# Optimization experiments

Hardware: AMD Instinct MI355X
Metric: run time of the kernel (lower is better)

The kernel has to match this reference:

```python
import jax, jax.numpy as jnp
import numpy as np

N_NODES = 100000


def _gcn_conv(x, W, b, src, dst, n):
    # PyG GCNConv (default): add self-loops, norm = deg^{-1/2}[src] * deg^{-1/2}[dst]
    # degree computed on target nodes (col) with unit edge weights, then
    # out[i] = sum_{(j->i)} norm_ji * (x_j @ W) + b
    loops = jnp.arange(n, dtype=src.dtype)
    s = jnp.concatenate([src, loops])
    d = jnp.concatenate([dst, loops])
    deg = jax.ops.segment_sum(jnp.ones_like(d, dtype=x.dtype), d, num_segments=n)
    dinv = jnp.where(deg > 0, jax.lax.rsqrt(deg), 0.0)
    h = x @ W                                  # [n, out_dim]
    norm = (dinv[s] * dinv[d])[:, None]        # [E+n, 1]
    msg = h[s] * norm                          # gather + scale
    out = jax.ops.segment_sum(msg, d, num_segments=n)  # scatter-add to targets
    return out + b


def setup_inputs() -> dict:
    key = jax.random.key(0)
    ks = jax.random.split(key, 4)
    x = jax.random.normal(ks[0], (N_NODES, 128), dtype=jnp.float32)
    edge_index = jax.random.randint(ks[1], (2, 1600000), 0, N_NODES, dtype=jnp.int64)
    W1 = jax.random.normal(ks[2], (128, 16), dtype=jnp.float32) * (1.0 / np.sqrt(128))
    b1 = jnp.zeros((16,), dtype=jnp.float32)
    W2 = jax.random.normal(ks[3], (16, 3), dtype=jnp.float32) * (1.0 / np.sqrt(16))
    b2 = jnp.zeros((3,), dtype=jnp.float32)
    return {"x": x, "edge_index": edge_index, "W1": W1, "b1": b1, "W2": W2, "b2": b2}


def reference(x, edge_index, W1, b1, W2, b2):
    src, dst = edge_index[0], edge_index[1]
    n = x.shape[0]
    h = _gcn_conv(x, W1, b1, src, dst, n)
    h = jax.nn.relu(h)
    # F.dropout in eval mode == identity (deterministic baseline)
    h = _gcn_conv(h, W2, b2, src, dst, n)
    return jax.nn.log_softmax(h, axis=1)
```

## Files before the change

### kernel.cpp

```cpp
#include <hip/hip_runtime.h>
#include <hip/hip_fp16.h>
#include <math.h>


#define BSH 9
#define BNODES 512
#define P1 512

struct alignas(8) Half4 { __half x, y, z, w; };

__global__ void k1a_count(const int* __restrict__ dst, int* __restrict__ hist_t,
                          int NBK, int E) {
    __shared__ int lh[256];
    int t = threadIdx.x;
    lh[t] = 0;
    __syncthreads();
    int slice = (E + P1 - 1) / P1;
    int e0 = blockIdx.x * slice, e1 = min(E, e0 + slice);
    for (int e = e0 + t; e < e1; e += 256)
        atomicAdd(&lh[dst[e] >> BSH], 1);
    __syncthreads();
    for (int i = t; i < NBK; i += 256)
        hist_t[(size_t)i * P1 + blockIdx.x] = lh[i];
}

__global__ void kscan1(const int* __restrict__ hist_t, int* __restrict__ colpre_t,
                       int* __restrict__ btot, int NBK) {
    __shared__ int v[P1], part[256];
    int kb = blockIdx.x, t = threadIdx.x;
    v[t] = hist_t[(size_t)kb * P1 + t];
    v[t + 256] = hist_t[(size_t)kb * P1 + t + 256];
    __syncthreads();
    int a = v[2 * t], c = v[2 * t + 1];
    part[t] = a + c;
    __syncthreads();
    for (int o = 1; o < 256; o <<= 1) {
        int add = (t >= o) ? part[t - o] : 0;
        __syncthreads();
        part[t] += add;
        __syncthreads();
    }
    int pre = (t == 0) ? 0 : part[t - 1];
    colpre_t[(size_t)kb * P1 + 2 * t] = pre;
    colpre_t[(size_t)kb * P1 + 2 * t + 1] = pre + a;
    if (t == 255) btot[kb] = part[255];
}

__global__ void kscan2(const int* __restrict__ btot, int* __restrict__ bucket_base, int NBK) {
    __shared__ int s[256];
    int t = threadIdx.x;
    int orig = (t < NBK) ? btot[t] : 0;
    s[t] = orig;
    __syncthreads();
    for (int o = 1; o < 256; o <<= 1) {
        int add = (t >= o) ? s[t - o] : 0;
        __syncthreads();
        s[t] += add;
        __syncthreads();
    }
    if (t < NBK) {
        bucket_base[t] = s[t] - orig;
        if (t == NBK - 1) bucket_base[NBK] = s[t];
    }
}

__global__ void k1b_fat(const int* __restrict__ src, const int* __restrict__ dst,
                        const int* __restrict__ colpre_t, const int* __restrict__ bucket_base,
                        unsigned int* __restrict__ staging,
                        const float* __restrict__ x, const float* __restrict__ W1,
                        Half4* __restrict__ g1h, int NBK, int n, int E) {
    __shared__ float4 sW4[512];
    int b = blockIdx.x;
    if (b < P1) {
        int* loff = (int*)sW4;
        int* lcur = ((int*)sW4) + 1024;
        for (int i = threadIdx.x; i < NBK; i += 256) {
            loff[i] = bucket_base[i] + colpre_t[(size_t)i * P1 + b];
            lcur[i] = 0;
        }
        __syncthreads();
        int slice = (E + P1 - 1) / P1;
        int e0 = b * slice, e1 = min(E, e0 + slice);
        for (int e = e0 + threadIdx.x; e < e1; e += 256) {
            int d = dst[e], s = src[e];
            int k = d >> BSH;
            int t = atomicAdd(&lcur[k], 1);
            staging[loff[k] + t] = ((unsigned int)s << BSH) | (unsigned int)(d & (BNODES - 1));
        }
    } else {
        int tid = threadIdx.x;
        for (int i = tid; i < 512; i += 256) sW4[i] = ((const float4*)W1)[i];
        __syncthreads();
        int idx = (b - P1) * 256 + tid;
        int row = idx >> 2, c4 = idx & 3;
        if (row >= n) return;
        const float4* xr = (const float4*)(x + (size_t)row * 128);
        float4 acc = make_float4(0.f, 0.f, 0.f, 0.f);
        for (int q = 0; q < 32; ++q) {
            float4 xv = xr[q];
            #pragma unroll
            for (int j = 0; j < 4; ++j) {
                float s = (j == 0) ? xv.x : (j == 1) ? xv.y : (j == 2) ? xv.z : xv.w;
                float4 w = sW4[(q * 4 + j) * 4 + c4];
                acc.x += s * w.x; acc.y += s * w.y; acc.z += s * w.z; acc.w += s * w.w;
            }
        }
        Half4 h;
        h.x = __float2half(acc.x); h.y = __float2half(acc.y);
        h.z = __float2half(acc.z); h.w = __float2half(acc.w);
        g1h[(size_t)row * 4 + c4] = h;
    }
}

__global__ void __launch_bounds__(512) k2_bucket(
        const unsigned int* __restrict__ staging, const int* __restrict__ bucket_base,
        int* __restrict__ csr, int* __restrict__ deg, float* __restrict__ dinv,
        int* __restrict__ row_start, Half4* __restrict__ g1h, int n) {
    __shared__ int lh[BNODES], sc[BNODES], lcur[BNODES];
    __shared__ float ldv[BNODES];
    int kb = blockIdx.x, t = threadIdx.x;
    int node0 = kb << BSH;
    int nloc = min(BNODES, n - node0);
    int ebase = bucket_base[kb], ecnt = bucket_base[kb + 1] - ebase;
    lh[t] = 0; lcur[t] = 0;
    __syncthreads();
    for (int e = t; e < ecnt; e += 512)
        atomicAdd(&lh[staging[ebase + e] & (BNODES - 1)], 1);
    __syncthreads();
    int own = lh[t];
    sc[t] = own;
    __syncthreads();
    for (int o = 1; o < 512; o <<= 1) {
        int add = (t >= o) ? sc[t - o] : 0;
        __syncthreads();
        sc[t] += add;
        __syncthreads();
    }
    int excl = sc[t] - own;
    if (t < nloc) {
        deg[node0 + t] = own;
        row_start[node0 + t] = ebase + excl;
        float dv = rsqrtf((float)(own + 1));
        dinv[node0 + t] = dv;
        ldv[t] = dv;
    }
    sc[t] = excl;
    __syncthreads();
    for (int e = t; e < ecnt; e += 512) {
        unsigned int p = staging[ebase + e];
        int loc = p & (BNODES - 1);
        int s = (int)(p >> BSH);
        int tk = atomicAdd(&lcur[loc], 1);
        csr[ebase + sc[loc] + tk] = s;
    }
    for (int j = t; j < nloc * 4; j += 512) {
        float dv = ldv[j >> 2];
        Half4 v = g1h[(size_t)node0 * 4 + j];
        v.x = __float2half(__half2float(v.x) * dv);
        v.y = __float2half(__half2float(v.y) * dv);
        v.z = __float2half(__half2float(v.z) * dv);
        v.w = __float2half(__half2float(v.w) * dv);
        g1h[(size_t)node0 * 4 + j] = v;
    }
}

__global__ void k_gather1(const Half4* __restrict__ g1h, const int* __restrict__ csr,
                          const int* __restrict__ row_start, const int* __restrict__ deg,
                          const float* __restrict__ dinv, const float* __restrict__ b1,
                          const float* __restrict__ W2, Half4* __restrict__ g2h, int n) {
    int idx = blockIdx.x * 256 + threadIdx.x;
    int i = idx >> 4, t15 = idx & 15;
    if (i >= n) return;
    int esplit = t15 >> 2, c4 = t15 & 3;
    int off = row_start[i], dg = deg[i];
    float ax = 0.f, ay = 0.f, az = 0.f, aw = 0.f;
    if (esplit == 0) {
        Half4 sh = g1h[(size_t)i * 4 + c4];
        ax = __half2float(sh.x); ay = __half2float(sh.y);
        az = __half2float(sh.z); aw = __half2float(sh.w);
    }
    for (int k = esplit; k < dg; k += 4) {
        int s = csr[off + k];
        Half4 v = g1h[(size_t)s * 4 + c4];
        ax += __half2float(v.x); ay += __half2float(v.y);
        az += __half2float(v.z); aw += __half2float(v.w);
    }
    ax += __shfl_xor(ax, 4); ax += __shfl_xor(ax, 8);
    ay += __shfl_xor(ay, 4); ay += __shfl_xor(ay, 8);
    az += __shfl_xor(az, 4); az += __shfl_xor(az, 8);
    aw += __shfl_xor(aw, 4); aw += __shfl_xor(aw, 8);
    float di = dinv[i];
    float z0 = fmaxf(0.f, di * ax + b1[c4 * 4 + 0]);
    float z1 = fmaxf(0.f, di * ay + b1[c4 * 4 + 1]);
    float z2 = fmaxf(0.f, di * az + b1[c4 * 4 + 2]);
    float z3 = fmaxf(0.f, di * aw + b1[c4 * 4 + 3]);
    const float* w = W2 + c4 * 12;
    float o0 = z0 * w[0] + z1 * w[3] + z2 * w[6] + z3 * w[9];
    float o1 = z0 * w[1] + z1 * w[4] + z2 * w[7] + z3 * w[10];
    float o2 = z0 * w[2] + z1 * w[5] + z2 * w[8] + z3 * w[11];
    o0 += __shfl_xor(o0, 1); o0 += __shfl_xor(o0, 2);
    o1 += __shfl_xor(o1, 1); o1 += __shfl_xor(o1, 2);
    o2 += __shfl_xor(o2, 1); o2 += __shfl_xor(o2, 2);
    if (t15 == 0) {
        Half4 g;
        g.x = __float2half(di * o0); g.y = __float2half(di * o1);
        g.z = __float2half(di * o2); g.w = __float2half(0.f);
        g2h[i] = g;
    }
}

__global__ void k_gather2(const Half4* __restrict__ g2h, const int* __restrict__ csr,
                          const int* __restrict__ row_start, const int* __restrict__ deg,
                          const float* __restrict__ dinv, const float* __restrict__ b2,
                          float* __restrict__ out, int n) {
    int idx = blockIdx.x * 256 + threadIdx.x;
    int i = idx >> 4, l = idx & 15;
    if (i >= n) return;
    int off = row_start[i], dg = deg[i];
    float v0 = 0.f, v1 = 0.f, v2 = 0.f;
    if (l == 0) {
        Half4 s = g2h[i];
        v0 = __half2float(s.x); v1 = __half2float(s.y); v2 = __half2float(s.z);
    }
    for (int e = l; e < dg; e += 16) {
        int s = csr[off + e];
        Half4 g = g2h[s];
        v0 += __half2float(g.x); v1 += __half2float(g.y); v2 += __half2float(g.z);
    }
    #pragma unroll
    for (int o = 1; o < 16; o <<= 1) {
        v0 += __shfl_xor(v0, o);
        v1 += __shfl_xor(v1, o);
        v2 += __shfl_xor(v2, o);
    }
    if (l >= 3) return;
    float di = dinv[i];
    float a0 = di * v0 + b2[0];
    float a1 = di * v1 + b2[1];
    float a2 = di * v2 + b2[2];
    float m = fmaxf(a0, fmaxf(a1, a2));
    float lse = logf(expf(a0 - m) + expf(a1 - m) + expf(a2 - m));
    float r = (l == 0) ? a0 : (l == 1) ? a1 : a2;
    out[(size_t)i * 3 + l] = r - m - lse;
}

extern "C" void kernel_launch(void* const* d_in, const int* in_sizes, int n_in,
                              void* d_out, int out_size, void* d_ws, size_t ws_size,
                              hipStream_t stream) {
    const float* x  = (const float*)d_in[0];
    const int*   ei = (const int*)d_in[1];
    const float* W1 = (const float*)d_in[2];
    const float* b1 = (const float*)d_in[3];
    const float* W2 = (const float*)d_in[4];
    const float* b2 = (const float*)d_in[5];
    float* out = (float*)d_out;

    const int n = in_sizes[0] / 128;
    const int E = in_sizes[1] / 2;
    const int* src = ei;
    const int* dst = ei + E;

    const int NBK = (n + BNODES - 1) >> BSH;

    auto align = [](size_t v) { return (v + 255) & ~(size_t)255; };
    char* ws = (char*)d_ws;
    size_t o = 0;
    int* hist_t      = (int*)(ws + o); o = align(o + (size_t)NBK * P1 * 4);
    int* colpre_t    = (int*)(ws + o); o = align(o + (size_t)NBK * P1 * 4);
    int* btot        = (int*)(ws + o); o = align(o + (size_t)NBK * 4);
    int* bucket_base = (int*)(ws + o); o = align(o + (size_t)(NBK + 1) * 4);
    int* deg         = (int*)(ws + o); o = align(o + (size_t)n * 4);
    float* dinv      = (float*)(ws + o); o = align(o + (size_t)n * 4);
    int* row_start   = (int*)(ws + o); o = align(o + (size_t)n * 4);
    unsigned int* staging = (unsigned int*)(ws + o); o = align(o + (size_t)E * 4);
    int* csr         = (int*)(ws + o); o = align(o + (size_t)E * 4);
    Half4* g1h       = (Half4*)(ws + o); o = align(o + (size_t)n * 4 * 8);
    Half4* g2h       = (Half4*)(ws + o); o = align(o + (size_t)n * 8);

    const int B = 256;
    int gn4  = (4 * n + B - 1) / B;
    int gn16 = (16 * n + B - 1) / B;

    k1a_count<<<P1, B, 0, stream>>>(dst, hist_t, NBK, E);
    kscan1<<<NBK, B, 0, stream>>>(hist_t, colpre_t, btot, NBK);
    kscan2<<<1, B, 0, stream>>>(btot, bucket_base, NBK);
    k1b_fat<<<P1 + gn4, B, 0, stream>>>(src, dst, colpre_t, bucket_base, staging,
                                        x, W1, g1h, NBK, n, E);
    k2_bucket<<<NBK, 512, 0, stream>>>(staging, bucket_base, csr, deg, dinv, row_start,
                                       g1h, n);
    k_gather1<<<gn16, B, 0, stream>>>(g1h, csr, row_start, deg, dinv, b1, W2, g2h, n);
    k_gather2<<<gn16, B, 0, stream>>>(g2h, csr, row_start, deg, dinv, b2, out, n);
}
```

Baseline: 182.8 us.

## Stage x tiles in LDS for GEMM, widen bucket blocks, 16-edge-parallel gather1

The dense x@W1 part of k1b_fat now loads a 64-row tile of x into padded shared memory with coalesced float4 loads before computing, instead of each thread reading its own row strided from global memory. k2_bucket runs with 1024 threads per block and guards the 512-entry scan. k_gather1 now has each of 16 lanes handle different edges and load the full 16-half row as two uint4s, then reduces 16 accumulators across lanes with shuffles. The cost is more registers and shuffles in gather1, plus extra shared memory use in k1b_fat.

New measurement: 182.0 us. No clear change (-0.4%).

```diff
diff --git a/kernel.cpp b/kernel.cpp
--- a/kernel.cpp
+++ b/kernel.cpp
@@ -6,6 +6,7 @@
 #define BSH 9
 #define BNODES 512
 #define P1 512
+#define GROWS 64
 
 struct alignas(8) Half4 { __half x, y, z, w; };
 
@@ -69,11 +70,12 @@
                         unsigned int* __restrict__ staging,
                         const float* __restrict__ x, const float* __restrict__ W1,
                         Half4* __restrict__ g1h, int NBK, int n, int E) {
+    __shared__ float sx[GROWS * 132];
     __shared__ float4 sW4[512];
     int b = blockIdx.x;
     if (b < P1) {
-        int* loff = (int*)sW4;
-        int* lcur = ((int*)sW4) + 1024;
+        int* loff = (int*)sx;
+        int* lcur = ((int*)sx) + 1024;
         for (int i = threadIdx.x; i < NBK; i += 256) {
             loff[i] = bucket_base[i] + colpre_t[(size_t)i * P1 + b];
             lcur[i] = 0;
@@ -88,16 +90,24 @@
             staging[loff[k] + t] = ((unsigned int)s << BSH) | (unsigned int)(d & (BNODES - 1));
         }
     } else {
-        int tid = threadIdx.x;
-        for (int i = tid; i < 512; i += 256) sW4[i] = ((const float4*)W1)[i];
-        __syncthreads();
-        int idx = (b - P1) * 256 + tid;
-        int row = idx >> 2, c4 = idx & 3;
+        int t = threadIdx.x;
+        int base = (b - P1) * GROWS;
+        for (int i = t; i < 512; i += 256) sW4[i] = ((const float4*)W1)[i];
+        for (int i = t; i < GROWS * 32; i += 256) {
+            int r = i >> 5, c = i & 31;
+            int row = base + r;
+            float4 v = (row < n) ? ((const float4*)x)[(size_t)row * 32 + c]
+                                 : make_float4(0.f, 0.f, 0.f, 0.f);
+            *((float4*)&sx[r * 132 + c * 4]) = v;
+        }
+        __syncthreads();
+        int r = t >> 2, c4 = t & 3;
+        int row = base + r;
         if (row >= n) return;
-        const float4* xr = (const float4*)(x + (size_t)row * 128);
         float4 acc = make_float4(0.f, 0.f, 0.f, 0.f);
+        #pragma unroll 8
         for (int q = 0; q < 32; ++q) {
-            float4 xv = xr[q];
+            float4 xv = *((const float4*)&sx[r * 132 + q * 4]);
             #pragma unroll
             for (int j = 0; j < 4; ++j) {
                 float s = (j == 0) ? xv.x : (j == 1) ? xv.y : (j == 2) ? xv.z : xv.w;
@@ -112,7 +122,7 @@
     }
 }
 
-__global__ void __launch_bounds__(512) k2_bucket(
+__global__ void __launch_bounds__(1024) k2_bucket(
         const unsigned int* __restrict__ staging, const int* __restrict__ bucket_base,
         int* __restrict__ csr, int* __restrict__ deg, float* __restrict__ dinv,
         int* __restrict__ row_start, Half4* __restrict__ g1h, int n) {
@@ -122,38 +132,41 @@
     int node0 = kb << BSH;
     int nloc = min(BNODES, n - node0);
     int ebase = bucket_base[kb], ecnt = bucket_base[kb + 1] - ebase;
-    lh[t] = 0; lcur[t] = 0;
-    __syncthreads();
-    for (int e = t; e < ecnt; e += 512)
+    if (t < BNODES) { lh[t] = 0; lcur[t] = 0; }
+    __syncthreads();
+    for (int e = t; e < ecnt; e += 1024)
         atomicAdd(&lh[staging[ebase + e] & (BNODES - 1)], 1);
     __syncthreads();
-    int own = lh[t];
-    sc[t] = own;
-    __syncthreads();
-    for (int o = 1; o < 512; o <<= 1) {
-        int add = (t >= o) ? sc[t - o] : 0;
-        __syncthreads();
-        sc[t] += add;
-        __syncthreads();
-    }
-    int excl = sc[t] - own;
-    if (t < nloc) {
-        deg[node0 + t] = own;
-        row_start[node0 + t] = ebase + excl;
-        float dv = rsqrtf((float)(own + 1));
-        dinv[node0 + t] = dv;
-        ldv[t] = dv;
-    }
-    sc[t] = excl;
-    __syncthreads();
-    for (int e = t; e < ecnt; e += 512) {
+    int own = 0;
+    if (t < BNODES) { own = lh[t]; sc[t] = own; }
+    __syncthreads();
+    for (int o = 1; o < BNODES; o <<= 1) {
+        int add = 0;
+        if (t < BNODES && t >= o) add = sc[t - o];
+        __syncthreads();
+        if (t < BNODES) sc[t] += add;
+        __syncthreads();
+    }
+    if (t < BNODES) {
+        int excl = sc[t] - own;
+        if (t < nloc) {
+            deg[node0 + t] = own;
+            row_start[node0 + t] = ebase + excl;
+            float dv = rsqrtf((float)(own + 1));
+            dinv[node0 + t] = dv;
+            ldv[t] = dv;
+        }
+        sc[t] = excl;
+    }
+    __syncthreads();
+    for (int e = t; e < ecnt; e += 1024) {
         unsigned int p = staging[ebase + e];
         int loc = p & (BNODES - 1);
         int s = (int)(p >> BSH);
         int tk = atomicAdd(&lcur[loc], 1);
         csr[ebase + sc[loc] + tk] = s;
     }
-    for (int j = t; j < nloc * 4; j += 512) {
+    for (int j = t; j < nloc * 4; j += 1024) {
         float dv = ldv[j >> 2];
         Half4 v = g1h[(size_t)node0 * 4 + j];
         v.x = __float2half(__half2float(v.x) * dv);
@@ -164,49 +177,61 @@
     }
 }
 
-__global__ void k_gather1(const Half4* __restrict__ g1h, const int* __restrict__ csr,
+__global__ void k_gather1(const uint4* __restrict__ g1q, const int* __restrict__ csr,
                           const int* __restrict__ row_start, const int* __restrict__ deg,
                           const float* __restrict__ dinv, const float* __restrict__ b1,
                           const float* __restrict__ W2, Half4* __restrict__ g2h, int n) {
     int idx = blockIdx.x * 256 + threadIdx.x;
-    int i = idx >> 4, t15 = idx & 15;
+    int i = idx >> 4, l = idx & 15;
     if (i >= n) return;
-    int esplit = t15 >> 2, c4 = t15 & 3;
     int off = row_start[i], dg = deg[i];
-    float ax = 0.f, ay = 0.f, az = 0.f, aw = 0.f;
-    if (esplit == 0) {
-        Half4 sh = g1h[(size_t)i * 4 + c4];
-        ax = __half2float(sh.x); ay = __half2float(sh.y);
-        az = __half2float(sh.z); aw = __half2float(sh.w);
-    }
-    for (int k = esplit; k < dg; k += 4) {
+    float acc[16];
+    #pragma unroll
+    for (int j = 0; j < 16; ++j) acc[j] = 0.f;
+    if (l == 0) {
+        uint4 p0 = g1q[2 * (size_t)i], p1 = g1q[2 * (size_t)i + 1];
+        const __half2* h0 = reinterpret_cast<const __half2*>(&p0);
+        const __half2* h1 = reinterpret_cast<const __half2*>(&p1);
+        #pragma unroll
+        for (int j = 0; j < 4; ++j) {
+            float2 f0 = __half22float2(h0[j]);
+            float2 f1 = __half22float2(h1[j]);
+            acc[2 * j] += f0.x; acc[2 * j + 1] += f0.y;
+            acc[8 + 2 * j] += f1.x; acc[9 + 2 * j] += f1.y;
+        }
+    }
+    for (int k = l; k < dg; k += 16) {
         int s = csr[off + k];
-        Half4 v = g1h[(size_t)s * 4 + c4];
-        ax += __half2float(v.x); ay += __half2float(v.y);
-        az += __half2float(v.z); aw += __half2float(v.w);
-    }
-    ax += __shfl_xor(ax, 4); ax += __shfl_xor(ax, 8);
-    ay += __shfl_xor(ay, 4); ay += __shfl_xor(ay, 8);
-    az += __shfl_xor(az, 4); az += __shfl_xor(az, 8);
-    aw += __shfl_xor(aw, 4); aw += __shfl_xor(aw, 8);
+        uint4 p0 = g1q[2 * (size_t)s], p1 = g1q[2 * (size_t)s + 1];
+        const __half2* h0 = reinterpret_cast<const __half2*>(&p0);
+        const __half2* h1 = reinterpret_cast<const __half2*>(&p1);
+        #pragma unroll
+        for (int j = 0; j < 4; ++j) {
+            float2 f0 = __half22float2(h0[j]);
+            float2 f1 = __half22float2(h1[j]);
+            acc[2 * j] += f0.x; acc[2 * j + 1] += f0.y;
+            acc[8 + 2 * j] += f1.x; acc[9 + 2 * j] += f1.y;
+        }
+    }
+    #pragma unroll
+    for (int m = 1; m < 16; m <<= 1) {
+        #pragma unroll
+        for (int j = 0; j < 16; ++j) acc[j] += __shfl_xor(acc[j], m);
+    }
+    if (l != 0) return;
     float di = dinv[i];
-    float z0 = fmaxf(0.f, di * ax + b1[c4 * 4 + 0]);
-    float z1 = fmaxf(0.f, di * ay + b1[c4 * 4 + 1]);
-    float z2 = fmaxf(0.f, di * az + b1[c4 * 4 + 2]);
-    float z3 = fmaxf(0.f, di * aw + b1[c4 * 4 + 3]);
-    const float* w = W2 + c4 * 12;
-    float o0 = z0 * w[0] + z1 * w[3] + z2 * w[6] + z3 * w[9];
-    float o1 = z0 * w[1] + z1 * w[4] + z2 * w[7] + z3 * w[10];
-    float o2 = z0 * w[2] + z1 * w[5] + z2 * w[8] + z3 * w[11];
-    o0 += __shfl_xor(o0, 1); o0 += __shfl_xor(o0, 2);
-    o1 += __shfl_xor(o1, 1); o1 += __shfl_xor(o1, 2);
-    o2 += __shfl_xor(o2, 1); o2 += __shfl_xor(o2, 2);
-    if (t15 == 0) {
-        Half4 g;
-        g.x = __float2half(di * o0); g.y = __float2half(di * o1);
-        g.z = __float2half(di * o2); g.w = __float2half(0.f);
-        g2h[i] = g;
-    }
+    float o0 = 0.f, o1 = 0.f, o2 = 0.f;
+    #pragma unroll
+    for (int c = 0; c < 16; ++c) {
+        float z = fmaxf(0.f, di * acc[c] + b1[c]);
+        o0 += z * W2[c * 3 + 0];
+        o1 += z * W2[c * 3 + 1];
+        o2 += z * W2[c * 3 + 2];
+    }
+    Half4 g;
+    g.x = __float2half(di * o0); g.y = __float2half(di * o1);
+    g.z = __float2half(di * o2); g.w = __float2half(0.f);
+    g2h[i] = g;
 }
 
 __global__ void k_gather2(const Half4* __restrict__ g2h, const int* __restrict__ csr,
@@ -278,16 +303,17 @@
     Half4* g2h       = (Half4*)(ws + o); o = align(o + (size_t)n * 8);
 
     const int B = 256;
-    int gn4  = (4 * n + B - 1) / B;
-    int gn16 = (16 * n + B - 1) / B;
+    int gGemm = (n + GROWS - 1) / GROWS;
+    int gn16  = (16 * n + B - 1) / B;
 
     k1a_count<<<P1, B, 0, stream>>>(dst, hist_t, NBK, E);
     kscan1<<<NBK, B, 0, stream>>>(hist_t, colpre_t, btot, NBK);
     kscan2<<<1, B, 0, stream>>>(btot, bucket_base, NBK);
-    k1b_fat<<<P1 + gn4, B, 0, stream>>>(src, dst, colpre_t, bucket_base, staging,
-                                        x, W1, g1h, NBK, n, E);
-    k2_bucket<<<NBK, 512, 0, stream>>>(staging, bucket_base, csr, deg, dinv, row_start,
-                                       g1h, n);
-    k_gather1<<<gn16, B, 0, stream>>>(g1h, csr, row_start, deg, dinv, b1, W2, g2h, n);
+    k1b_fat<<<P1 + gGemm, B, 0, stream>>>(src, dst, colpre_t, bucket_base, staging,
+                                          x, W1, g1h, NBK, n, E);
+    k2_bucket<<<NBK, 1024, 0, stream>>>(staging, bucket_base, csr, deg, dinv, row_start,
+                                        g1h, n);
+    k_gather1<<<gn16, B, 0, stream>>>((const uint4*)g1h, csr, row_start, deg, dinv, b1, W2,
+                                      g2h, n);
     k_gather2<<<gn16, B, 0, stream>>>(g2h, csr, row_start, deg, dinv, b2, out, n);
 }
```
